# Kernel tuning notes

Hardware: AMD Instinct MI355X
Metric: run time of the kernel (lower is better)

## Reference

```python
import jax, jax.numpy as jnp
import numpy as np

WS = 8            # window_size
N = WS * WS       # tokens per window = 64
C = 512           # dim
TEMB = 512        # temb_dim
H = 8             # num_heads
D = C // H        # head_dim = 64
B = 2048          # number of windows (batch * windows per image)


def _rel_pos_index(ws: int) -> np.ndarray:
    coords = np.stack(np.meshgrid(np.arange(ws), np.arange(ws), indexing='ij'))  # (2, ws, ws)
    flat = coords.reshape(2, -1)                      # (2, N)
    rel = flat[:, :, None] - flat[:, None, :]         # (2, N, N)
    rel = rel.transpose(1, 2, 0).copy()               # (N, N, 2)
    rel[:, :, 0] += ws - 1
    rel[:, :, 1] += ws - 1
    rel[:, :, 0] *= 2 * ws - 1
    return rel.sum(-1)                                # (N, N) int

_RP_INDEX = jnp.asarray(_rel_pos_index(WS))           # (N, N)


def setup_inputs() -> dict:
    key = jax.random.key(0)
    ks = jax.random.split(key, 8)
    std = 0.02
    return {
        'x': jax.random.normal(ks[0], (B, N, C), dtype=jnp.float32),
        'temb': jax.random.normal(ks[1], (B, TEMB), dtype=jnp.float32),
        'w_qkv': jax.random.normal(ks[2], (C, 3 * C), dtype=jnp.float32) * std,
        'b_qkv': jnp.zeros((3 * C,), dtype=jnp.float32),
        'w_qkv_t': jax.random.normal(ks[3], (TEMB, 3 * C), dtype=jnp.float32) * std,
        'w_proj': jax.random.normal(ks[4], (C, C), dtype=jnp.float32) * std,
        'b_proj': jnp.zeros((C,), dtype=jnp.float32),
        'rpb_table': jax.random.normal(ks[5], ((2 * WS - 1) ** 2, H), dtype=jnp.float32) * std,
    }


def reference(x, temb, w_qkv, b_qkv, w_qkv_t, w_proj, b_proj, rpb_table):
    # x: (B, N, C), temb: (B, TEMB)
    scale = D ** (-0.5)
    qkv = x @ w_qkv + b_qkv + (temb @ w_qkv_t)[:, None, :]     # (B, N, 3C)
    qkv = qkv.reshape(x.shape[0], N, 3, H, D)
    q = qkv[:, :, 0].transpose(0, 2, 1, 3)                      # (B, H, N, D)
    k = qkv[:, :, 1].transpose(0, 2, 1, 3)
    v = qkv[:, :, 2].transpose(0, 2, 1, 3)
    attn = jnp.einsum('bhnd,bhmd->bhnm', q * scale, k)          # (B, H, N, N)
    bias = rpb_table[_RP_INDEX]                                 # (N, N, H)
    attn = attn + bias.transpose(2, 0, 1)[None]                 # + (1, H, N, N)
    attn = jax.nn.softmax(attn, axis=-1)
    out = jnp.einsum('bhnm,bhmd->bhnd', attn, v)                # (B, H, N, D)
    out = out.transpose(0, 2, 1, 3).reshape(x.shape[0], N, C)   # (B, N, C)
    return out @ w_proj + b_proj
```

## Files before the change

kernel.cpp:

```cpp
#include <hip/hip_runtime.h>

typedef __bf16 bf16;
typedef __bf16 bf16x4 __attribute__((ext_vector_type(4)));
typedef __bf16 bf16x8 __attribute__((ext_vector_type(8)));
typedef float f32x4 __attribute__((ext_vector_type(4)));

#define MFMA(a, b, c) __builtin_amdgcn_mfma_f32_16x16x32_bf16((a), (b), (c), 0, 0, 0)

__global__ void transpose_cast(const float* __restrict__ in, bf16* __restrict__ out,
                               int R, int C) {
  int i = blockIdx.x * 256 + threadIdx.x;
  if (i >= R * C) return;
  int r = i / C, c = i - r * C;
  out[(size_t)c * R + r] = (bf16)in[i];
}

template <bool AF32>
__global__ __launch_bounds__(256) void gemm_bt_bias(
    const void* __restrict__ Ap, const bf16* __restrict__ Bt,
    const float* __restrict__ bias, float* __restrict__ C,
    int M, int N, int K) {
  __shared__ bf16 lA[128 * 32];
  __shared__ bf16 lB[128 * 32];
  const int t = threadIdx.x, l = t & 63;
  const int w = t >> 6, wr = w >> 1, wc = w & 1;
  const int li = l & 15, kl = (l >> 4) << 3;
  const long bm0 = (long)blockIdx.x * 128, bn0 = (long)blockIdx.y * 128;
  f32x4 acc[4][4] = {};
  for (int ks = 0; ks < (K >> 5); ++ks) {
    const int k0 = ks << 5;
    __syncthreads();
#pragma unroll
    for (int i = 0; i < 2; ++i) {
      int u = t + (i << 8);
      int row = u >> 2, kc = (u & 3) << 3;
      if constexpr (AF32) {
        const float* ag = (const float*)Ap + (bm0 + row) * K + k0 + kc;
        f32x4 v0 = *((const f32x4*)ag);
        f32x4 v1 = *((const f32x4*)(ag + 4));
        bf16x8 pk;
        pk[0] = (bf16)v0[0]; pk[1] = (bf16)v0[1]; pk[2] = (bf16)v0[2]; pk[3] = (bf16)v0[3];
        pk[4] = (bf16)v1[0]; pk[5] = (bf16)v1[1]; pk[6] = (bf16)v1[2]; pk[7] = (bf16)v1[3];
        *((bf16x8*)&lA[u << 3]) = pk;
      } else {
        *((bf16x8*)&lA[u << 3]) =
            *((const bf16x8*)((const bf16*)Ap + (bm0 + row) * K + k0 + kc));
      }
      *((bf16x8*)&lB[u << 3]) = *((const bf16x8*)&Bt[(bn0 + row) * K + k0 + kc]);
    }
    __syncthreads();
    bf16x8 af[4], bfr[4];
#pragma unroll
    for (int mt = 0; mt < 4; ++mt)
      af[mt] = *((const bf16x8*)&lA[(wr * 64 + mt * 16 + li) * 32 + kl]);
#pragma unroll
    for (int nt = 0; nt < 4; ++nt)
      bfr[nt] = *((const bf16x8*)&lB[(wc * 64 + nt * 16 + li) * 32 + kl]);
#pragma unroll
    for (int mt = 0; mt < 4; ++mt)
#pragma unroll
      for (int nt = 0; nt < 4; ++nt)
        acc[mt][nt] = MFMA(af[mt], bfr[nt], acc[mt][nt]);
  }
#pragma unroll
  for (int mt = 0; mt < 4; ++mt)
#pragma unroll
    for (int nt = 0; nt < 4; ++nt) {
      long col = bn0 + wc * 64 + nt * 16 + li;
      float bv = bias[col];
#pragma unroll
      for (int r = 0; r < 4; ++r) {
        long row = bm0 + wr * 64 + mt * 16 + ((l >> 4) << 2) + r;
        C[row * N + col] = acc[mt][nt][r] + bv;
      }
    }
}

__global__ __launch_bounds__(512) void fused_qkv_attn(
    const float* __restrict__ x, const bf16* __restrict__ w1t,
    const float* __restrict__ tbias, const float* __restrict__ rpb,
    bf16* __restrict__ attn_out) {
  __shared__ bf16 xs[64 * 520];
  __shared__ float ts[1536];
  __shared__ bf16 qs[2][64 * 72];
  __shared__ bf16 kts[2][64 * 72];
  __shared__ bf16 vts[2][64 * 72];

  const int b = blockIdx.x;
  const int t = threadIdx.x, l = t & 63, w = t >> 6;
  const int li = l & 15, lg = l >> 4, kl = lg << 3;
  const int strip = w & 3, hl = w >> 2;

  {
    const float* xb = x + (size_t)b * (64 * 512);
#pragma unroll
    for (int i = 0; i < 16; ++i) {
      int f4 = t + (i << 9);
      int n = f4 >> 7, c4 = (f4 & 127) << 2;
      f32x4 v = *((const f32x4*)&xb[n * 512 + c4]);
      bf16x4 pk;
      pk[0] = (bf16)v[0]; pk[1] = (bf16)v[1]; pk[2] = (bf16)v[2]; pk[3] = (bf16)v[3];
      *((bf16x4*)&xs[n * 520 + c4]) = pk;
    }
    const float* tb = tbias + (size_t)b * 1536;
    for (int i = t; i < 1536; i += 512) ts[i] = tb[i];
  }

  int chh[3], csec[3], cdc[3];
#pragma unroll
  for (int ct = 0; ct < 3; ++ct) {
    int lc = 48 * w + 16 * ct;
    int hh = lc >= 192;
    chh[ct] = hh;
    csec[ct] = (lc - 192 * hh) >> 6;
    cdc[ct] = lc & 63;
  }

  int rpidx[4][4];
#pragma unroll
  for (int ct = 0; ct < 4; ++ct)
#pragma unroll
    for (int r = 0; r < 4; ++r) {
      int n = 16 * strip + (lg << 2) + r, m = 16 * ct + li;
      rpidx[ct][r] = (((n >> 3) - (m >> 3) + 7) * 15 + ((n & 7) - (m & 7) + 7)) * 8;
    }
  __syncthreads();

  for (int hp = 0; hp < 4; ++hp) {
    f32x4 acc[3][4] = {};
    int j0[3];
#pragma unroll
    for (int ct = 0; ct < 3; ++ct)
      j0[ct] = csec[ct] * 512 + (hp * 2 + chh[ct]) * 64 + cdc[ct];
#pragma unroll 4
    for (int ks = 0; ks < 16; ++ks) {
      int k0 = ks << 5;
      bf16x8 af[4];
#pragma unroll
      for (int mt = 0; mt < 4; ++mt)
        af[mt] = *((const bf16x8*)&xs[(mt * 16 + li) * 520 + k0 + kl]);
#pragma unroll
      for (int ct = 0; ct < 3; ++ct) {
        bf16x8 bw = *((const bf16x8*)&w1t[(size_t)(j0[ct] + li) * 512 + k0 + kl]);
#pragma unroll
        for (int mt = 0; mt < 4; ++mt)
          acc[ct][mt] = MFMA(af[mt], bw, acc[ct][mt]);
      }
    }
#pragma unroll
    for (int ct = 0; ct < 3; ++ct) {
      int hh = chh[ct], sec = csec[ct], dc = cdc[ct];
      float tb = ts[j0[ct] + li];
#pragma unroll
      for (int mt = 0; mt < 4; ++mt) {
        int row0 = mt * 16 + (lg << 2);
        if (sec == 0) {
#pragma unroll
          for (int r = 0; r < 4; ++r)
            qs[hh][(row0 + r) * 72 + dc + li] = (bf16)((acc[ct][mt][r] + tb) * 0.125f);
        } else if (sec == 1) {
#pragma unroll
          for (int r = 0; r < 4; ++r)
            kts[hh][(row0 + r) * 72 + dc + li] = (bf16)(acc[ct][mt][r] + tb);
        } else {
          bf16x4 pk;
#pragma unroll
          for (int r = 0; r < 4; ++r) pk[r] = (bf16)(acc[ct][mt][r] + tb);
          *((bf16x4*)&vts[hh][(dc + li) * 72 + row0]) = pk;
        }
      }
    }
    __syncthreads();

    f32x4 accS[4] = {};
#pragma unroll
    for (int kk = 0; kk < 2; ++kk) {
      bf16x8 aq = *((const bf16x8*)&qs[hl][(16 * strip + li) * 72 + kk * 32 + kl]);
#pragma unroll
      for (int ct = 0; ct < 4; ++ct) {
        bf16x8 bk = *((const bf16x8*)&kts[hl][(16 * ct + li) * 72 + kk * 32 + kl]);
        accS[ct] = MFMA(aq, bk, accS[ct]);
      }
    }
    const int h = hp * 2 + hl;
    const float* rpbh = rpb + h;
    float sv[4][4], rsum[4];
#pragma unroll
    for (int ct = 0; ct < 4; ++ct)
#pragma unroll
      for (int r = 0; r < 4; ++r)
        sv[ct][r] = accS[ct][r] + rpbh[rpidx[ct][r]];
#pragma unroll
    for (int r = 0; r < 4; ++r) {
      float m = fmaxf(fmaxf(sv[0][r], sv[1][r]), fmaxf(sv[2][r], sv[3][r]));
      m = fmaxf(m, __shfl_xor(m, 1));
      m = fmaxf(m, __shfl_xor(m, 2));
      m = fmaxf(m, __shfl_xor(m, 4));
      m = fmaxf(m, __shfl_xor(m, 8));
      float s = 0.f;
#pragma unroll
      for (int ct = 0; ct < 4; ++ct) {
        float p = __expf(sv[ct][r] - m);
        sv[ct][r] = p;
        s += p;
      }
      s += __shfl_xor(s, 1);
      s += __shfl_xor(s, 2);
      s += __shfl_xor(s, 4);
      s += __shfl_xor(s, 8);
      rsum[r] = s;
    }
#pragma unroll
    for (int ct = 0; ct < 4; ++ct)
#pragma unroll
      for (int r = 0; r < 4; ++r)
        qs[hl][(16 * strip + (lg << 2) + r) * 72 + 16 * ct + li] = (bf16)sv[ct][r];

    f32x4 accO[4] = {};
#pragma unroll
    for (int kk = 0; kk < 2; ++kk) {
      bf16x8 ap = *((const bf16x8*)&qs[hl][(16 * strip + li) * 72 + kk * 32 + kl]);
#pragma unroll
      for (int ct = 0; ct < 4; ++ct) {
        bf16x8 bv = *((const bf16x8*)&vts[hl][(16 * ct + li) * 72 + kk * 32 + kl]);
        accO[ct] = MFMA(ap, bv, accO[ct]);
      }
    }
    bf16* ob = attn_out + (size_t)b * (64 * 512) + h * 64;
    float rinv[4];
#pragma unroll
    for (int r = 0; r < 4; ++r) rinv[r] = 1.0f / rsum[r];
#pragma unroll
    for (int ct = 0; ct < 4; ++ct)
#pragma unroll
      for (int r = 0; r < 4; ++r)
        ob[(size_t)(16 * strip + (lg << 2) + r) * 512 + 16 * ct + li] =
            (bf16)(accO[ct][r] * rinv[r]);
    __syncthreads();
  }
}

extern "C" void kernel_launch(void* const* d_in, const int* in_sizes, int n_in,
                              void* d_out, int out_size, void* d_ws, size_t ws_size,
                              hipStream_t stream) {
  (void)in_sizes; (void)n_in; (void)out_size; (void)ws_size;
  const float* x       = (const float*)d_in[0];
  const float* temb    = (const float*)d_in[1];
  const float* w_qkv   = (const float*)d_in[2];
  const float* b_qkv   = (const float*)d_in[3];
  const float* w_qkv_t = (const float*)d_in[4];
  const float* w_proj  = (const float*)d_in[5];
  const float* b_proj  = (const float*)d_in[6];
  const float* rpb     = (const float*)d_in[7];
  float* out = (float*)d_out;

  char* ws = (char*)d_ws;
  size_t off = 0;
  auto take = [&](size_t bytes) {
    void* p = ws + off;
    off += (bytes + 255) & ~(size_t)255;
    return p;
  };
  bf16* w1t  = (bf16*)take((size_t)1536 * 512 * 2);
  bf16* w3t  = (bf16*)take((size_t)1536 * 512 * 2);
  bf16* w2t  = (bf16*)take((size_t)512 * 512 * 2);
  float* tb  = (float*)take((size_t)2048 * 1536 * 4);
  bf16* attn = (bf16*)take((size_t)131072 * 512 * 2);

  transpose_cast<<<(512 * 1536 + 255) / 256, 256, 0, stream>>>(w_qkv, w1t, 512, 1536);
  transpose_cast<<<(512 * 1536 + 255) / 256, 256, 0, stream>>>(w_qkv_t, w3t, 512, 1536);
  transpose_cast<<<(512 * 512 + 255) / 256, 256, 0, stream>>>(w_proj, w2t, 512, 512);

  gemm_bt_bias<true><<<dim3(2048 / 128, 1536 / 128), 256, 0, stream>>>(
      temb, w3t, b_qkv, tb, 2048, 1536, 512);

  fused_qkv_attn<<<2048, 512, 0, stream>>>(x, w1t, tb, rpb, attn);

  gemm_bt_bias<false><<<dim3(131072 / 128, 512 / 128), 256, 0, stream>>>(
      attn, w2t, b_proj, out, 131072, 512, 512);
}
```

Baseline: 757.8 us.

## Stream x through double-buffered LDS k-slices to cut fused kernel LDS footprint

The fused QKV+attention kernel no longer keeps the whole 64x512 bf16 x tile plus the temb-bias row resident in LDS. It streams x in 64-wide k-slices through a small double buffer. On the first head pair it converts fp32 x to bf16 and writes a bf16 copy to global memory; later passes reload that copy with direct global-to-LDS loads. This shrinks LDS so more workgroups fit per CU (launch bounds now ask for 4), at the cost of re-reading x four times, an extra bf16 write of x, more barriers, and temb-bias loads straight from global memory.

```diff
diff --git a/kernel.cpp b/kernel.cpp
--- a/kernel.cpp
+++ b/kernel.cpp
@@ -6,6 +6,11 @@
 typedef float f32x4 __attribute__((ext_vector_type(4)));
 
 #define MFMA(a, b, c) __builtin_amdgcn_mfma_f32_16x16x32_bf16((a), (b), (c), 0, 0, 0)
+
+__device__ __forceinline__ void gload16(const void* g, void* l) {
+  __builtin_amdgcn_global_load_lds((const __attribute__((address_space(1))) void*)g,
+                                   (__attribute__((address_space(3))) void*)l, 16, 0, 0);
+}
 
 __global__ void transpose_cast(const float* __restrict__ in, bf16* __restrict__ out,
                                int R, int C) {
@@ -76,12 +81,11 @@
     }
 }
 
-__global__ __launch_bounds__(512) void fused_qkv_attn(
-    const float* __restrict__ x, const bf16* __restrict__ w1t,
-    const float* __restrict__ tbias, const float* __restrict__ rpb,
-    bf16* __restrict__ attn_out) {
-  __shared__ bf16 xs[64 * 520];
-  __shared__ float ts[1536];
+__global__ __launch_bounds__(512, 4) void fused_qkv_attn(
+    const float* __restrict__ x, bf16* __restrict__ xb,
+    const bf16* __restrict__ w1t, const float* __restrict__ tbias,
+    const float* __restrict__ rpb, bf16* __restrict__ attn_out) {
+  __shared__ bf16 xt[2][4096];
   __shared__ bf16 qs[2][64 * 72];
   __shared__ bf16 kts[2][64 * 72];
   __shared__ bf16 vts[2][64 * 72];
@@ -91,20 +95,9 @@
   const int li = l & 15, lg = l >> 4, kl = lg << 3;
   const int strip = w & 3, hl = w >> 2;
 
-  {
-    const float* xb = x + (size_t)b * (64 * 512);
-#pragma unroll
-    for (int i = 0; i < 16; ++i) {
-      int f4 = t + (i << 9);
-      int n = f4 >> 7, c4 = (f4 & 127) << 2;
-      f32x4 v = *((const f32x4*)&xb[n * 512 + c4]);
-      bf16x4 pk;
-      pk[0] = (bf16)v[0]; pk[1] = (bf16)v[1]; pk[2] = (bf16)v[2]; pk[3] = (bf16)v[3];
-      *((bf16x4*)&xs[n * 520 + c4]) = pk;
-    }
-    const float* tb = tbias + (size_t)b * 1536;
-    for (int i = t; i < 1536; i += 512) ts[i] = tb[i];
-  }
+  const size_t xoff = ((size_t)b * 64 + (t & 63)) * 512 + ((t >> 6) << 3);
+  bf16* const ldsw0 = &xt[0][(size_t)w * 512];
+  bf16* const ldsw1 = &xt[1][(size_t)w * 512];
 
   int chh[3], csec[3], cdc[3];
 #pragma unroll
@@ -124,36 +117,69 @@
       int n = 16 * strip + (lg << 2) + r, m = 16 * ct + li;
       rpidx[ct][r] = (((n >> 3) - (m >> 3) + 7) * 15 + ((n & 7) - (m & 7) + 7)) * 8;
     }
+
+  auto stage = [&](int pp, int ks, int nb) {
+    const int k0 = ks << 6;
+    if (pp == 0) {
+      f32x4 v0 = *((const f32x4*)(x + xoff + k0));
+      f32x4 v1 = *((const f32x4*)(x + xoff + k0 + 4));
+      bf16x8 pk;
+      pk[0] = (bf16)v0[0]; pk[1] = (bf16)v0[1]; pk[2] = (bf16)v0[2]; pk[3] = (bf16)v0[3];
+      pk[4] = (bf16)v1[0]; pk[5] = (bf16)v1[1]; pk[6] = (bf16)v1[2]; pk[7] = (bf16)v1[3];
+      *((bf16x8*)&xt[nb][t * 8]) = pk;
+      *((bf16x8*)(xb + xoff + k0)) = pk;
+    } else {
+      gload16(xb + xoff + k0, nb ? ldsw1 : ldsw0);
+    }
+  };
+
+  stage(0, 0, 0);
   __syncthreads();
-
-  for (int hp = 0; hp < 4; ++hp) {
+  int cb = 0;
+
+  for (int p = 0; p < 4; ++p) {
+    int j0[3];
+    const bf16* wrow[3];
+#pragma unroll
+    for (int ct = 0; ct < 3; ++ct) {
+      j0[ct] = csec[ct] * 512 + (p * 2 + chh[ct]) * 64 + cdc[ct];
+      wrow[ct] = w1t + (size_t)(j0[ct] + li) * 512;
+    }
     f32x4 acc[3][4] = {};
-    int j0[3];
-#pragma unroll
-    for (int ct = 0; ct < 3; ++ct)
-      j0[ct] = csec[ct] * 512 + (hp * 2 + chh[ct]) * 64 + cdc[ct];
-#pragma unroll 4
-    for (int ks = 0; ks < 16; ++ks) {
-      int k0 = ks << 5;
-      bf16x8 af[4];
-#pragma unroll
-      for (int mt = 0; mt < 4; ++mt)
-        af[mt] = *((const bf16x8*)&xs[(mt * 16 + li) * 520 + k0 + kl]);
-#pragma unroll
-      for (int ct = 0; ct < 3; ++ct) {
-        bf16x8 bw = *((const bf16x8*)&w1t[(size_t)(j0[ct] + li) * 512 + k0 + kl]);
+
+    for (int ks = 0; ks < 8; ++ks) {
+      {
+        int pn = p, ksn = ks + 1;
+        if (ksn == 8) { pn = p + 1; ksn = 0; }
+        if (!(p == 3 && ks == 7)) stage(pn, ksn, cb ^ 1);
+      }
+      const int k0 = ks << 6;
+#pragma unroll
+      for (int kk = 0; kk < 2; ++kk) {
+        bf16x8 af[4];
 #pragma unroll
         for (int mt = 0; mt < 4; ++mt)
-          acc[ct][mt] = MFMA(af[mt], bw, acc[ct][mt]);
-      }
-    }
+          af[mt] = *((const bf16x8*)&xt[cb][((kk * 4 + lg) * 64 + mt * 16 + li) * 8]);
+#pragma unroll
+        for (int ct = 0; ct < 3; ++ct) {
+          bf16x8 bw = *((const bf16x8*)(wrow[ct] + k0 + kk * 32 + kl));
+#pragma unroll
+          for (int mt = 0; mt < 4; ++mt)
+            acc[ct][mt] = MFMA(af[mt], bw, acc[ct][mt]);
+        }
+      }
+      __syncthreads();
+      cb ^= 1;
+    }
+
+    const float* tbp = tbias + (size_t)b * 1536;
 #pragma unroll
     for (int ct = 0; ct < 3; ++ct) {
-      int hh = chh[ct], sec = csec[ct], dc = cdc[ct];
-      float tb = ts[j0[ct] + li];
+      const int hh = chh[ct], sec = csec[ct], dc = cdc[ct];
+      const float tb = tbp[j0[ct] + li];
 #pragma unroll
       for (int mt = 0; mt < 4; ++mt) {
-        int row0 = mt * 16 + (lg << 2);
+        const int row0 = mt * 16 + (lg << 2);
         if (sec == 0) {
 #pragma unroll
           for (int r = 0; r < 4; ++r)
@@ -182,7 +208,7 @@
         accS[ct] = MFMA(aq, bk, accS[ct]);
       }
     }
-    const int h = hp * 2 + hl;
+    const int h = p * 2 + hl;
     const float* rpbh = rpb + h;
     float sv[4][4], rsum[4];
 #pragma unroll
@@ -200,9 +226,9 @@
       float s = 0.f;
 #pragma unroll
       for (int ct = 0; ct < 4; ++ct) {
-        float p = __expf(sv[ct][r] - m);
-        sv[ct][r] = p;
-        s += p;
+        float pxv = __expf(sv[ct][r] - m);
+        sv[ct][r] = pxv;
+        s += pxv;
       }
       s += __shfl_xor(s, 1);
       s += __shfl_xor(s, 2);
@@ -266,6 +292,7 @@
   bf16* w2t  = (bf16*)take((size_t)512 * 512 * 2);
   float* tb  = (float*)take((size_t)2048 * 1536 * 4);
   bf16* attn = (bf16*)take((size_t)131072 * 512 * 2);
+  bf16* xb   = (bf16*)take((size_t)131072 * 512 * 2);
 
   transpose_cast<<<(512 * 1536 + 255) / 256, 256, 0, stream>>>(w_qkv, w1t, 512, 1536);
   transpose_cast<<<(512 * 1536 + 255) / 256, 256, 0, stream>>>(w_qkv_t, w3t, 512, 1536);
@@ -274,7 +301,7 @@
   gemm_bt_bias<true><<<dim3(2048 / 128, 1536 / 128), 256, 0, stream>>>(
       temb, w3t, b_qkv, tb, 2048, 1536, 512);
 
-  fused_qkv_attn<<<2048, 512, 0, stream>>>(x, w1t, tb, rpb, attn);
+  fused_qkv_attn<<<2048, 512, 0, stream>>>(x, xb, w1t, tb, rpb, attn);
 
   gemm_bt_bias<false><<<dim3(131072 / 128, 512 / 128), 256, 0, stream>>>(
       attn, w2t, b_proj, out, 131072, 512, 512);
```

New measurement: 861.2 us. 1.14x slower.
